# Kernel optimization log

Hardware: AMD Instinct MI355X
Metric: run time of the kernel (lower is better)

Reference implementation:

```python
import jax, jax.numpy as jnp
import numpy as np

N = 100000
E = 3200000
F_IN = 128
H1, C1 = 2, 16          # conv1: heads=2, out_channels=16, concat -> 32
H2, C2 = 1, 40          # conv2: heads=1, out_channels=num_classes=40
NEG_SLOPE = 0.2


def setup_inputs() -> dict:
    key = jax.random.key(0)
    ks = jax.random.split(key, 12)
    features = jax.random.normal(ks[0], (N, F_IN), dtype=jnp.float32)
    edges = jax.random.randint(ks[1], (2, E), 0, N, dtype=jnp.int64)
    weight = jax.random.uniform(ks[2], (E,), dtype=jnp.float32)  # ignored (edge_dim=None)
    s = 0.1
    W1 = jax.random.normal(ks[3], (F_IN, H1 * C1), dtype=jnp.float32) * s
    att_src1 = jax.random.normal(ks[4], (H1, C1), dtype=jnp.float32) * s
    att_dst1 = jax.random.normal(ks[5], (H1, C1), dtype=jnp.float32) * s
    b1 = jnp.zeros((H1 * C1,), dtype=jnp.float32)
    W2 = jax.random.normal(ks[6], (H1 * C1, H2 * C2), dtype=jnp.float32) * s
    att_src2 = jax.random.normal(ks[7], (H2, C2), dtype=jnp.float32) * s
    att_dst2 = jax.random.normal(ks[8], (H2, C2), dtype=jnp.float32) * s
    b2 = jnp.zeros((H2 * C2,), dtype=jnp.float32)
    return {"features": features, "edges": edges, "weight": weight,
            "W1": W1, "att_src1": att_src1, "att_dst1": att_dst1, "b1": b1,
            "W2": W2, "att_src2": att_src2, "att_dst2": att_dst2, "b2": b2}


def _segment_softmax(e, seg, num_segments):
    # e: [E, H]; softmax over edges sharing the same destination node
    m = jax.ops.segment_max(e, seg, num_segments=num_segments)
    ex = jnp.exp(e - m[seg])
    s = jax.ops.segment_sum(ex, seg, num_segments=num_segments)
    return ex / (s[seg] + 1e-16)


def _gat_conv(x, src, dst, W, att_src, att_dst, bias, heads, out_ch):
    n = x.shape[0]
    h = (x @ W).reshape(n, heads, out_ch)                  # [N,H,C]
    a_src = jnp.sum(h * att_src, axis=-1)                  # [N,H]
    a_dst = jnp.sum(h * att_dst, axis=-1)                  # [N,H]
    e = a_src[src] + a_dst[dst]                            # [E,H]
    e = jnp.where(e > 0, e, NEG_SLOPE * e)                 # LeakyReLU(0.2)
    alpha = _segment_softmax(e, dst, n)                    # [E,H]
    msg = h[src] * alpha[:, :, None]                       # [E,H,C]
    out = jax.ops.segment_sum(msg, dst, num_segments=n)    # [N,H,C]
    return out.reshape(n, heads * out_ch) + bias           # concat=True


def reference(features, edges, weight, W1, att_src1, att_dst1, b1,
              W2, att_src2, att_dst2, b2):
    n = features.shape[0]
    # GATConv default add_self_loops=True (self-loop removal of pre-existing
    # loops skipped: negligible for random edges and not jit-shape-friendly)
    loop = jnp.arange(n, dtype=edges.dtype)
    src = jnp.concatenate([edges[0], loop])
    dst = jnp.concatenate([edges[1], loop])
    x = _gat_conv(features, src, dst, W1, att_src1, att_dst1, b1, H1, C1)
    x = jax.nn.relu(x)
    # F.dropout with training=self.training -> identity in eval mode
    x = _gat_conv(x, src, dst, W2, att_src2, att_dst2, b2, H2, C2)
    return x
```

## Files before the change

### kernel.cpp

```cpp
#include <hip/hip_runtime.h>


#define DEVFN __device__ __forceinline__
#define CB_SHIFT 9
#define CB_SZ 512
#define CHUNK 8192
#define A2B 240

DEVFN unsigned short f2h(float f) {
  _Float16 h = (_Float16)f;
  unsigned short u;
  __builtin_memcpy(&u, &h, 2);
  return u;
}
DEVFN float h2f(unsigned short u) {
  _Float16 h;
  __builtin_memcpy(&h, &u, 2);
  return (float)h;
}

DEVFN float lrelu(float e) { return e > 0.f ? e : 0.2f * e; }

DEVFN void acc8(float* acc, float x, uint4 u) {
  acc[0] = fmaf(x, h2f(u.x & 0xffff), acc[0]);
  acc[1] = fmaf(x, h2f(u.x >> 16),    acc[1]);
  acc[2] = fmaf(x, h2f(u.y & 0xffff), acc[2]);
  acc[3] = fmaf(x, h2f(u.y >> 16),    acc[3]);
  acc[4] = fmaf(x, h2f(u.z & 0xffff), acc[4]);
  acc[5] = fmaf(x, h2f(u.z >> 16),    acc[5]);
  acc[6] = fmaf(x, h2f(u.w & 0xffff), acc[6]);
  acc[7] = fmaf(x, h2f(u.w >> 16),    acc[7]);
}

DEVFN void read_edge(const long long* eg64, const int* eg32, int is64, int E,
                     int i, int& s, int& d) {
  if (i >= E) { s = d = i - E; return; }
  if (is64) { s = (int)eg64[i]; d = (int)eg64[E + i]; }
  else      { s = eg32[i];      d = eg32[E + i]; }
}

DEVFN int detect64(const int* eg32, int E, int i0, int t) {
  int base = i0;
  if (base > E - 64) base = E - 64;
  if (base < 0) base = 0;
  int i = base + (t & 63);
  unsigned long long m = __ballot((i < E) && (eg32[2 * i + 1] != 0));
  return m == 0ull;
}

__global__ void scan_blocks(const int* __restrict__ cnt, int* __restrict__ rp,
                            int* __restrict__ bsum, int n) {
  __shared__ int buf[2][1024];
  int t = threadIdx.x;
  int gid = blockIdx.x * 1024 + t;
  int v = (gid < n) ? cnt[gid] : 0;
  buf[0][t] = v;
  __syncthreads();
  int pin = 0;
  for (int offd = 1; offd < 1024; offd <<= 1) {
    int nv = buf[pin][t];
    if (t >= offd) nv += buf[pin][t - offd];
    buf[1 - pin][t] = nv;
    pin = 1 - pin;
    __syncthreads();
  }
  int inc = buf[pin][t];
  if (gid < n) rp[gid] = inc - v;
  if (t == 1023) bsum[blockIdx.x] = inc;
}

__global__ void scan_sums(const int* bsum, int* boff, int nb) {
  if (blockIdx.x == 0 && threadIdx.x == 0) {
    int r = 0;
    for (int i = 0; i < nb; i++) { boff[i] = r; r += bsum[i]; }
  }
}

__global__ void scan_add(int* rp, const int* boff, int n, int total) {
  int i = blockIdx.x * 1024 + threadIdx.x;
  if (i < n) rp[i] = rp[i] + boff[blockIdx.x];
  if (i == 0) rp[n] = total;
}

__global__ __launch_bounds__(256) void chunk_hist(const long long* eg64,
                                                  const int* eg32,
                                                  int E, int N, int NWG,
                                                  int* __restrict__ histg) {
  __shared__ int lh[CB_SZ];
  int w = blockIdx.x, t = threadIdx.x;
  int NB2 = (N + CB_SZ - 1) / CB_SZ;
  for (int j = t; j < NB2; j += 256) lh[j] = 0;
  int i0 = w * CHUNK;
  int is64 = detect64(eg32, E, i0, t);
  __syncthreads();
  int EN = E + N;
  int i1 = i0 + CHUNK; if (i1 > EN) i1 = EN;
  for (int i = i0 + t; i < i1; i += 256) {
    int d;
    if (i >= E) d = i - E;
    else d = is64 ? (int)eg64[E + i] : eg32[E + i];
    atomicAdd(&lh[d >> CB_SHIFT], 1);
  }
  __syncthreads();
  for (int b = t; b < NB2; b += 256) histg[b * NWG + w] = lh[b];
}

__global__ __launch_bounds__(256) void chunk_scatter(const long long* eg64,
                                                     const int* eg32,
                                                     int E, int N, int NWG,
                                                     const int* __restrict__ hists,
                                                     int* __restrict__ tmp) {
  __shared__ int lcur[CB_SZ];
  int w = blockIdx.x, t = threadIdx.x;
  int NB2 = (N + CB_SZ - 1) / CB_SZ;
  for (int b = t; b < NB2; b += 256) lcur[b] = hists[b * NWG + w];
  int i0 = w * CHUNK;
  int is64 = detect64(eg32, E, i0, t);
  __syncthreads();
  int EN = E + N;
  int i1 = i0 + CHUNK; if (i1 > EN) i1 = EN;
  for (int i = i0 + t; i < i1; i += 256) {
    int s, d;
    read_edge(eg64, eg32, is64, E, i, s, d);
    int b = d >> CB_SHIFT;
    int pos = atomicAdd(&lcur[b], 1);
    tmp[pos] = (s << CB_SHIFT) | (d & (CB_SZ - 1));
  }
}

__global__ __launch_bounds__(256) void bucket_rp_sort(const int* __restrict__ hists,
                                                      int NWG,
                                                      const int* __restrict__ tmp,
                                                      int* __restrict__ rp,
                                                      int* __restrict__ csr,
                                                      int N, int EN) {
  __shared__ int lc[CB_SZ];
  __shared__ int ps[256];
  __shared__ int lcur[CB_SZ];
  int b = blockIdx.x, t = threadIdx.x;
  for (int j = t; j < CB_SZ; j += 256) lc[j] = 0;
  __syncthreads();
  int w0 = hists[b * NWG];
  int w1 = hists[(b + 1) * NWG];
  for (int p = w0 + t; p < w1; p += 256)
    atomicAdd(&lc[tmp[p] & (CB_SZ - 1)], 1);
  __syncthreads();
  int a = lc[2 * t], c = lc[2 * t + 1];
  ps[t] = a + c;
  __syncthreads();
  for (int off = 1; off < 256; off <<= 1) {
    int v = ps[t];
    int u = (t >= off) ? ps[t - off] : 0;
    __syncthreads();
    ps[t] = v + u;
    __syncthreads();
  }
  int base = w0 + ps[t] - (a + c);
  lcur[2 * t] = base;
  lcur[2 * t + 1] = base + a;
  int n0 = b * CB_SZ;
  if (n0 + 2 * t < N) rp[n0 + 2 * t] = base;
  if (n0 + 2 * t + 1 < N) rp[n0 + 2 * t + 1] = base + a;
  if (b == (int)gridDim.x - 1 && t == 0) rp[N] = EN;
  __syncthreads();
  for (int p = w0 + t; p < w1; p += 256) {
    int e = tmp[p];
    int pos = atomicAdd(&lcur[e & (CB_SZ - 1)], 1);
    csr[pos] = e >> CB_SHIFT;
  }
}

__global__ __launch_bounds__(256) void gemm1f(const float* __restrict__ X,
                                              const float* __restrict__ W,
                                              const float* __restrict__ att_s,
                                              const float* __restrict__ att_d,
                                              uint4* __restrict__ h1h,
                                              float* __restrict__ as1,
                                              float* __restrict__ ad1, int N) {
  __shared__ float Wl[128 * 32];
  __shared__ float Asl[32], Adl[32];
  int t = threadIdx.x;
  for (int i = t; i < 1024; i += 256)
    ((float4*)Wl)[i] = ((const float4*)W)[i];
  if (t < 32) { Asl[t] = att_s[t]; Adl[t] = att_d[t]; }
  __syncthreads();
  int n = blockIdx.x * 256 + t;
  if (n >= N) return;
  const float4* X4 = (const float4*)(X + (size_t)n * 128);
  float acc[32];
#pragma unroll
  for (int c = 0; c < 32; c++) acc[c] = 0.f;
  for (int k4 = 0; k4 < 32; k4++) {
    float4 x = X4[k4];
    const float4* w4 = (const float4*)(Wl + k4 * 128);
#pragma unroll
    for (int c4 = 0; c4 < 8; c4++) {
      float4 w0 = w4[c4], w1 = w4[8 + c4], w2 = w4[16 + c4], w3 = w4[24 + c4];
      float* A = acc + c4 * 4;
      A[0] = fmaf(x.x, w0.x, A[0]); A[1] = fmaf(x.x, w0.y, A[1]);
      A[2] = fmaf(x.x, w0.z, A[2]); A[3] = fmaf(x.x, w0.w, A[3]);
      A[0] = fmaf(x.y, w1.x, A[0]); A[1] = fmaf(x.y, w1.y, A[1]);
      A[2] = fmaf(x.y, w1.z, A[2]); A[3] = fmaf(x.y, w1.w, A[3]);
      A[0] = fmaf(x.z, w2.x, A[0]); A[1] = fmaf(x.z, w2.y, A[1]);
      A[2] = fmaf(x.z, w2.z, A[2]); A[3] = fmaf(x.z, w2.w, A[3]);
      A[0] = fmaf(x.w, w3.x, A[0]); A[1] = fmaf(x.w, w3.y, A[1]);
      A[2] = fmaf(x.w, w3.z, A[2]); A[3] = fmaf(x.w, w3.w, A[3]);
    }
  }
  float s0 = 0.f, d0 = 0.f, s1 = 0.f, d1 = 0.f;
#pragma unroll
  for (int c = 0; c < 16; c++) {
    s0 = fmaf(acc[c], Asl[c], s0);
    d0 = fmaf(acc[c], Adl[c], d0);
    s1 = fmaf(acc[16 + c], Asl[16 + c], s1);
    d1 = fmaf(acc[16 + c], Adl[16 + c], d1);
  }
  as1[n * 2] = s0; as1[n * 2 + 1] = s1;
  ad1[n * 2] = d0; ad1[n * 2 + 1] = d1;
#pragma unroll
  for (int j = 0; j < 4; j++) {
    uint4 u;
    u.x = (unsigned)f2h(acc[j * 8 + 0]) | ((unsigned)f2h(acc[j * 8 + 1]) << 16);
    u.y = (unsigned)f2h(acc[j * 8 + 2]) | ((unsigned)f2h(acc[j * 8 + 3]) << 16);
    u.z = (unsigned)f2h(acc[j * 8 + 4]) | ((unsigned)f2h(acc[j * 8 + 5]) << 16);
    u.w = (unsigned)f2h(acc[j * 8 + 6]) | ((unsigned)f2h(acc[j * 8 + 7]) << 16);
    h1h[(size_t)n * 4 + j] = u;
  }
}

__global__ __launch_bounds__(256, 8) void agg1_gemm2(
    const int* __restrict__ rp, const int* __restrict__ csr,
    const float* __restrict__ as, const float* __restrict__ ad,
    const uint4* __restrict__ h1h, const float* __restrict__ b1,
    const float* __restrict__ W2, const float* __restrict__ as2w,
    const float* __restrict__ ad2w, uint4* __restrict__ h2h,
    float* __restrict__ as2, float* __restrict__ ad2, int N) {
  __shared__ float Wl[32 * 40];
  __shared__ float As2l[40], Ad2l[40];
  __shared__ float x1t[16][33];
  __shared__ float h2r[16][41];
  int t = threadIdx.x;
  for (int i = t; i < 320; i += 256)
    ((float4*)Wl)[i] = ((const float4*)W2)[i];
  if (t < 40) { As2l[t] = as2w[t]; Ad2l[t] = ad2w[t]; }
  int nl = t >> 4, r = t & 15;
  int half = r >> 2, cq = r & 3;
  int h = cq >> 1;
  int n = blockIdx.x * 16 + nl;
  float acc[8] = {0, 0, 0, 0, 0, 0, 0, 0};
  float ssum = 0.f;
  if (n < N) {
    int p0 = rp[n], p1 = rp[n + 1];
    float adv = ad[n * 2 + h];
    int p = p0 + half;
    for (; p + 12 < p1; p += 16) {
      int sA = csr[p], sB = csr[p + 4], sC = csr[p + 8], sD = csr[p + 12];
      float eA = as[sA * 2 + h] + adv;
      float eB = as[sB * 2 + h] + adv;
      float eC = as[sC * 2 + h] + adv;
      float eD = as[sD * 2 + h] + adv;
      uint4 uA = h1h[(size_t)sA * 4 + cq];
      uint4 uB = h1h[(size_t)sB * 4 + cq];
      uint4 uC = h1h[(size_t)sC * 4 + cq];
      uint4 uD = h1h[(size_t)sD * 4 + cq];
      float xA = __expf(lrelu(eA));
      float xB = __expf(lrelu(eB));
      float xC = __expf(lrelu(eC));
      float xD = __expf(lrelu(eD));
      ssum += (xA + xB) + (xC + xD);
      acc8(acc, xA, uA);
      acc8(acc, xB, uB);
      acc8(acc, xC, uC);
      acc8(acc, xD, uD);
    }
    if (p < p1) {
      bool vB = p + 4 < p1, vC = p + 8 < p1;
      int pB = vB ? p + 4 : p;
      int pC = vC ? p + 8 : p;
      int sA = csr[p], sB = csr[pB], sC = csr[pC];
      float eA = as[sA * 2 + h] + adv;
      float eB = as[sB * 2 + h] + adv;
      float eC = as[sC * 2 + h] + adv;
      uint4 uA = h1h[(size_t)sA * 4 + cq];
      uint4 uB = h1h[(size_t)sB * 4 + cq];
      uint4 uC = h1h[(size_t)sC * 4 + cq];
      float xA = __expf(lrelu(eA));
      float xB = vB ? __expf(lrelu(eB)) : 0.f;
      float xC = vC ? __expf(lrelu(eC)) : 0.f;
      ssum += xA + xB + xC;
      acc8(acc, xA, uA);
      acc8(acc, xB, uB);
      acc8(acc, xC, uC);
    }
  }
#pragma unroll
  for (int j = 0; j < 8; j++) acc[j] += __shfl_xor(acc[j], 4);
  ssum += __shfl_xor(ssum, 4);
#pragma unroll
  for (int j = 0; j < 8; j++) acc[j] += __shfl_xor(acc[j], 8);
  ssum += __shfl_xor(ssum, 8);
  if (n < N && half == 0) {
    float inv = 1.0f / (ssum + 1e-16f);
    float4 ba = ((const float4*)b1)[cq * 2];
    float4 bb = ((const float4*)b1)[cq * 2 + 1];
    int ch0 = cq * 8;
    x1t[nl][ch0 + 0] = fmaxf(fmaf(acc[0], inv, ba.x), 0.f);
    x1t[nl][ch0 + 1] = fmaxf(fmaf(acc[1], inv, ba.y), 0.f);
    x1t[nl][ch0 + 2] = fmaxf(fmaf(acc[2], inv, ba.z), 0.f);
    x1t[nl][ch0 + 3] = fmaxf(fmaf(acc[3], inv, ba.w), 0.f);
    x1t[nl][ch0 + 4] = fmaxf(fmaf(acc[4], inv, bb.x), 0.f);
    x1t[nl][ch0 + 5] = fmaxf(fmaf(acc[5], inv, bb.y), 0.f);
    x1t[nl][ch0 + 6] = fmaxf(fmaf(acc[6], inv, bb.z), 0.f);
    x1t[nl][ch0 + 7] = fmaxf(fmaf(acc[7], inv, bb.w), 0.f);
  }
  __syncthreads();
  if (n < N && r < 8) {
    float acc2[5] = {0, 0, 0, 0, 0};
    int cb = r * 5;
    for (int k = 0; k < 32; k++) {
      float x = x1t[nl][k];
#pragma unroll
      for (int c = 0; c < 5; c++)
        acc2[c] = fmaf(x, Wl[k * 40 + cb + c], acc2[c]);
    }
    float ss = 0.f, sd = 0.f;
#pragma unroll
    for (int c = 0; c < 5; c++) {
      ss = fmaf(acc2[c], As2l[cb + c], ss);
      sd = fmaf(acc2[c], Ad2l[cb + c], sd);
    }
#pragma unroll
    for (int off = 1; off < 8; off <<= 1) {
      ss += __shfl_xor(ss, off);
      sd += __shfl_xor(sd, off);
    }
    if (r == 0) { as2[n] = ss; ad2[n] = sd; }
#pragma unroll
    for (int c = 0; c < 5; c++) h2r[nl][cb + c] = acc2[c];
  }
  __syncthreads();
  if (n < N && r < 5) {
    const float* hr = h2r[nl] + r * 8;
    uint4 u;
    u.x = (unsigned)f2h(hr[0]) | ((unsigned)f2h(hr[1]) << 16);
    u.y = (unsigned)f2h(hr[2]) | ((unsigned)f2h(hr[3]) << 16);
    u.z = (unsigned)f2h(hr[4]) | ((unsigned)f2h(hr[5]) << 16);
    u.w = (unsigned)f2h(hr[6]) | ((unsigned)f2h(hr[7]) << 16);
    h2h[(size_t)n * 8 + r] = u;
  }
}

__global__ __launch_bounds__(256, 8) void agg2_fused(const int* __restrict__ rp,
                                                     const int* __restrict__ csr,
                                                     const float* __restrict__ as,
                                                     const float* __restrict__ ad,
                                                     const uint4* __restrict__ h2h,
                                                     const float* __restrict__ bias,
                                                     float* __restrict__ outp, int N) {
  __shared__ float part[256][9];
  int t = threadIdx.x;
  int idx = blockIdx.x * A2B + t;
  bool act = (t < A2B) && (idx < N * 20);
  int n = 0, half = 0, cq = 0, p0 = 0, p1 = 0;
  float adv = 0.f;
  if (act) {
    n = idx / 20;
    int rr = idx % 20;
    half = rr / 5;
    cq = rr - half * 5;
    p0 = rp[n]; p1 = rp[n + 1];
    adv = ad[n];
  }
  float acc[8] = {0, 0, 0, 0, 0, 0, 0, 0};
  float ssum = 0.f;
  if (act) {
    int p = p0 + half;
    for (; p + 12 < p1; p += 16) {
      int sA = csr[p], sB = csr[p + 4], sC = csr[p + 8], sD = csr[p + 12];
      float eA = as[sA] + adv;
      float eB = as[sB] + adv;
      float eC = as[sC] + adv;
      float eD = as[sD] + adv;
      uint4 uA = h2h[(size_t)sA * 8 + cq];
      uint4 uB = h2h[(size_t)sB * 8 + cq];
      uint4 uC = h2h[(size_t)sC * 8 + cq];
      uint4 uD = h2h[(size_t)sD * 8 + cq];
      float xA = __expf(lrelu(eA));
      float xB = __expf(lrelu(eB));
      float xC = __expf(lrelu(eC));
      float xD = __expf(lrelu(eD));
      ssum += (xA + xB) + (xC + xD);
      acc8(acc, xA, uA);
      acc8(acc, xB, uB);
      acc8(acc, xC, uC);
      acc8(acc, xD, uD);
    }
    if (p < p1) {
      bool vB = p + 4 < p1, vC = p + 8 < p1;
      int pB = vB ? p + 4 : p;
      int pC = vC ? p + 8 : p;
      int sA = csr[p], sB = csr[pB], sC = csr[pC];
      float eA = as[sA] + adv;
      float eB = as[sB] + adv;
      float eC = as[sC] + adv;
      uint4 uA = h2h[(size_t)sA * 8 + cq];
      uint4 uB = h2h[(size_t)sB * 8 + cq];
      uint4 uC = h2h[(size_t)sC * 8 + cq];
      float xA = __expf(lrelu(eA));
      float xB = vB ? __expf(lrelu(eB)) : 0.f;
      float xC = vC ? __expf(lrelu(eC)) : 0.f;
      ssum += xA + xB + xC;
      acc8(acc, xA, uA);
      acc8(acc, xB, uB);
      acc8(acc, xC, uC);
    }
  }
  if (act && half) {
#pragma unroll
    for (int j = 0; j < 8; j++) part[t][j] = acc[j];
    part[t][8] = ssum;
  }
  __syncthreads();
  if (act && half == 0) {
#pragma unroll
    for (int j = 0; j < 8; j++)
      acc[j] += part[t + 5][j] + part[t + 10][j] + part[t + 15][j];
    ssum += part[t + 5][8] + part[t + 10][8] + part[t + 15][8];
    float inv = 1.0f / (ssum + 1e-16f);
    const float4* b4 = (const float4*)bias;
    float4 ba = b4[cq * 2], bb = b4[cq * 2 + 1];
    float4 r0, r1;
    r0.x = fmaf(acc[0], inv, ba.x);
    r0.y = fmaf(acc[1], inv, ba.y);
    r0.z = fmaf(acc[2], inv, ba.z);
    r0.w = fmaf(acc[3], inv, ba.w);
    r1.x = fmaf(acc[4], inv, bb.x);
    r1.y = fmaf(acc[5], inv, bb.y);
    r1.z = fmaf(acc[6], inv, bb.z);
    r1.w = fmaf(acc[7], inv, bb.w);
    ((float4*)outp)[(size_t)n * 10 + cq * 2]     = r0;
    ((float4*)outp)[(size_t)n * 10 + cq * 2 + 1] = r1;
  }
}

extern "C" void kernel_launch(void* const* d_in, const int* in_sizes, int n_in,
                              void* d_out, int out_size, void* d_ws, size_t ws_size,
                              hipStream_t stream) {
  const float* X    = (const float*)d_in[0];
  const long long* eg64 = (const long long*)d_in[1];
  const int* eg32   = (const int*)d_in[1];
  const float* W1   = (const float*)d_in[3];
  const float* as1w = (const float*)d_in[4];
  const float* ad1w = (const float*)d_in[5];
  const float* b1   = (const float*)d_in[6];
  const float* W2   = (const float*)d_in[7];
  const float* as2w = (const float*)d_in[8];
  const float* ad2w = (const float*)d_in[9];
  const float* b2   = (const float*)d_in[10];
  float* out = (float*)d_out;

  const int N  = in_sizes[0] / 128;
  const int E  = in_sizes[1] / 2;
  const int EN = E + N;
  const int NB2 = (N + CB_SZ - 1) / CB_SZ;
  const int NWG = (EN + CHUNK - 1) / CHUNK;
  const int NH  = NB2 * NWG;

  char* wbase = (char*)d_ws;
  size_t off = 0;
  auto alloc = [&](size_t bytes) -> void* {
    void* p = wbase + off;
    off += (bytes + 255) & ~(size_t)255;
    return p;
  };

  uint4* h1h = (uint4*)alloc((size_t)N * 64);
  uint4* h2h = (uint4*)alloc((size_t)N * 128);
  float* as1 = (float*)alloc((size_t)N * 2 * 4);
  float* ad1 = (float*)alloc((size_t)N * 2 * 4);
  float* as2 = (float*)alloc((size_t)N * 4);
  float* ad2 = (float*)alloc((size_t)N * 4);
  int* rp     = (int*)alloc((size_t)(N + 1) * 4);
  int* histg  = (int*)alloc((size_t)NH * 4);
  int* hists  = (int*)alloc((size_t)(NH + 1) * 4);
  int* bsum   = (int*)alloc(1024 * 4);
  int* boff   = (int*)alloc(1024 * 4);
  int* csr    = (int*)alloc((size_t)EN * 4);
  int* tmp    = (int*)alloc((size_t)EN * 4);
  (void)ws_size; (void)n_in; (void)out_size;

  const int gN  = (N + 255) / 256;
  const int nbH = (NH + 1023) / 1024;

  chunk_hist<<<NWG, 256, 0, stream>>>(eg64, eg32, E, N, NWG, histg);
  scan_blocks<<<nbH, 1024, 0, stream>>>(histg, hists, bsum, NH);
  scan_sums<<<1, 64, 0, stream>>>(bsum, boff, nbH);
  scan_add<<<nbH, 1024, 0, stream>>>(hists, boff, NH, EN);
  chunk_scatter<<<NWG, 256, 0, stream>>>(eg64, eg32, E, N, NWG, hists, tmp);
  bucket_rp_sort<<<NB2, 256, 0, stream>>>(hists, NWG, tmp, rp, csr, N, EN);

  gemm1f<<<gN, 256, 0, stream>>>(X, W1, as1w, ad1w, h1h, as1, ad1, N);
  agg1_gemm2<<<(N + 15) / 16, 256, 0, stream>>>(rp, csr, as1, ad1, h1h, b1,
                                                W2, as2w, ad2w, h2h, as2, ad2, N);
  agg2_fused<<<(N * 20 + A2B - 1) / A2B, 256, 0, stream>>>(rp, csr, as2, ad2,
                                                           h2h, b2, out, N);
}
```

Before: 367.8 us.

## Use finer CSR buckets and chunks, parallelize block-sum scan, alias tmp with h2h

Halves the destination bucket size to 256 nodes and shrinks edge chunks to 2048. This gives the histogram and scatter kernels about four times as many workgroups, and the per-bucket sort twice as many blocks with one node per thread. The serial single-thread scan of block sums becomes a 1024-thread parallel scan, because the histogram array and the number of block sums grow sharply. The temporary sort buffer now shares memory with the layer-2 feature buffer, since their lifetimes do not overlap, which shrinks the workspace footprint. The cost is a much larger histogram to write and scan, and less locality per chunk in the scatter.

```diff
diff --git a/kernel.cpp b/kernel.cpp
--- a/kernel.cpp
+++ b/kernel.cpp
@@ -2,9 +2,10 @@
 
 
 #define DEVFN __device__ __forceinline__
-#define CB_SHIFT 9
-#define CB_SZ 512
-#define CHUNK 8192
+#define CB_SHIFT 8
+#define CB_SZ 256
+#define CHUNK 2048
+#define HIST_MAX 512
 #define A2B 240
 
 DEVFN unsigned short f2h(float f) {
@@ -69,10 +70,29 @@
   if (t == 1023) bsum[blockIdx.x] = inc;
 }
 
-__global__ void scan_sums(const int* bsum, int* boff, int nb) {
-  if (blockIdx.x == 0 && threadIdx.x == 0) {
-    int r = 0;
-    for (int i = 0; i < nb; i++) { boff[i] = r; r += bsum[i]; }
+__global__ void scan_sums(const int* __restrict__ bsum, int* __restrict__ boff,
+                          int nb) {
+  __shared__ int buf[2][1024];
+  __shared__ int carry;
+  int t = threadIdx.x;
+  if (t == 0) carry = 0;
+  __syncthreads();
+  for (int base = 0; base < nb; base += 1024) {
+    int v = (base + t < nb) ? bsum[base + t] : 0;
+    buf[0][t] = v;
+    __syncthreads();
+    int pin = 0;
+    for (int off = 1; off < 1024; off <<= 1) {
+      int nv = buf[pin][t];
+      if (t >= off) nv += buf[pin][t - off];
+      buf[1 - pin][t] = nv;
+      pin = 1 - pin;
+      __syncthreads();
+    }
+    if (base + t < nb) boff[base + t] = carry + buf[pin][t] - v;
+    __syncthreads();
+    if (t == 0) carry += buf[pin][1023];
+    __syncthreads();
   }
 }
 
@@ -86,7 +106,7 @@
                                                   const int* eg32,
                                                   int E, int N, int NWG,
                                                   int* __restrict__ histg) {
-  __shared__ int lh[CB_SZ];
+  __shared__ int lh[HIST_MAX];
   int w = blockIdx.x, t = threadIdx.x;
   int NB2 = (N + CB_SZ - 1) / CB_SZ;
   for (int j = t; j < NB2; j += 256) lh[j] = 0;
@@ -110,7 +130,7 @@
                                                      int E, int N, int NWG,
                                                      const int* __restrict__ hists,
                                                      int* __restrict__ tmp) {
-  __shared__ int lcur[CB_SZ];
+  __shared__ int lcur[HIST_MAX];
   int w = blockIdx.x, t = threadIdx.x;
   int NB2 = (N + CB_SZ - 1) / CB_SZ;
   for (int b = t; b < NB2; b += 256) lcur[b] = hists[b * NWG + w];
@@ -138,15 +158,15 @@
   __shared__ int ps[256];
   __shared__ int lcur[CB_SZ];
   int b = blockIdx.x, t = threadIdx.x;
-  for (int j = t; j < CB_SZ; j += 256) lc[j] = 0;
+  lc[t] = 0;
   __syncthreads();
   int w0 = hists[b * NWG];
   int w1 = hists[(b + 1) * NWG];
   for (int p = w0 + t; p < w1; p += 256)
     atomicAdd(&lc[tmp[p] & (CB_SZ - 1)], 1);
   __syncthreads();
-  int a = lc[2 * t], c = lc[2 * t + 1];
-  ps[t] = a + c;
+  int a = lc[t];
+  ps[t] = a;
   __syncthreads();
   for (int off = 1; off < 256; off <<= 1) {
     int v = ps[t];
@@ -155,12 +175,10 @@
     ps[t] = v + u;
     __syncthreads();
   }
-  int base = w0 + ps[t] - (a + c);
-  lcur[2 * t] = base;
-  lcur[2 * t + 1] = base + a;
+  int base = w0 + ps[t] - a;
+  lcur[t] = base;
   int n0 = b * CB_SZ;
-  if (n0 + 2 * t < N) rp[n0 + 2 * t] = base;
-  if (n0 + 2 * t + 1 < N) rp[n0 + 2 * t + 1] = base + a;
+  if (n0 + t < N) rp[n0 + t] = base;
   if (b == (int)gridDim.x - 1 && t == 0) rp[N] = EN;
   __syncthreads();
   for (int p = w0 + t; p < w1; p += 256) {
@@ -475,7 +493,11 @@
   };
 
   uint4* h1h = (uint4*)alloc((size_t)N * 64);
-  uint4* h2h = (uint4*)alloc((size_t)N * 128);
+  size_t usz = (size_t)EN * 4;
+  if ((size_t)N * 128 > usz) usz = (size_t)N * 128;
+  char* uni = (char*)alloc(usz);
+  uint4* h2h = (uint4*)uni;
+  int*   tmp = (int*)uni;
   float* as1 = (float*)alloc((size_t)N * 2 * 4);
   float* ad1 = (float*)alloc((size_t)N * 2 * 4);
   float* as2 = (float*)alloc((size_t)N * 4);
@@ -486,7 +508,6 @@
   int* bsum   = (int*)alloc(1024 * 4);
   int* boff   = (int*)alloc(1024 * 4);
   int* csr    = (int*)alloc((size_t)EN * 4);
-  int* tmp    = (int*)alloc((size_t)EN * 4);
   (void)ws_size; (void)n_in; (void)out_size;
 
   const int gN  = (N + 255) / 256;
@@ -494,7 +515,7 @@
 
   chunk_hist<<<NWG, 256, 0, stream>>>(eg64, eg32, E, N, NWG, histg);
   scan_blocks<<<nbH, 1024, 0, stream>>>(histg, hists, bsum, NH);
-  scan_sums<<<1, 64, 0, stream>>>(bsum, boff, nbH);
+  scan_sums<<<1, 1024, 0, stream>>>(bsum, boff, nbH);
   scan_add<<<nbH, 1024, 0, stream>>>(hists, boff, NH, EN);
   chunk_scatter<<<NWG, 256, 0, stream>>>(eg64, eg32, E, N, NWG, hists, tmp);
   bucket_rp_sort<<<NB2, 256, 0, stream>>>(hists, NWG, tmp, rp, csr, N, EN);
```

Result: faster. 358.0 us (-2.7%).
